# Kernel optimization log

Measured on AMD Instinct MI355X. Metric: run time of the kernel, lower is better.

Reference implementation:

```python
import math
import jax, jax.numpy as jnp
import numpy as np

SHAPES = [(80, 80), (40, 40), (20, 20), (10, 10)]
BS, LQ, D, NH, NL, NP = 8, 1000, 256, 8, 4, 4
C = D // NH


def _offset_bias():
    # replicates _reset_parameters grid_init bias for sampling_offsets
    thetas = np.arange(NH, dtype=np.float32) * (2.0 * math.pi / NH)
    grid = np.stack([np.cos(thetas), np.sin(thetas)], -1)  # [NH,2]
    grid = grid / np.abs(grid).max(-1, keepdims=True)
    grid = np.tile(grid[:, None, None, :], (1, NL, NP, 1))  # [NH,NL,NP,2]
    for i in range(NP):
        grid[:, :, i, :] *= i + 1
    return jnp.asarray(grid.reshape(-1))


def setup_inputs() -> dict:
    key = jax.random.key(0)
    ks = jax.random.split(key, 8)
    len_v = sum(h * w for h, w in SHAPES)
    s = 1.0 / math.sqrt(D)
    starts = np.cumsum([0] + [h * w for h, w in SHAPES])[:-1]
    return {
        "query": jax.random.normal(ks[0], (BS, LQ, D), jnp.float32),
        "reference_points": jax.random.uniform(ks[1], (BS, LQ, NL, 2), jnp.float32),
        "value": jax.random.normal(ks[2], (BS, len_v, D), jnp.float32),
        "w_off": jax.random.normal(ks[3], (D, NH * NL * NP * 2), jnp.float32) * 0.01,
        "b_off": _offset_bias(),
        "w_attn": jax.random.normal(ks[4], (D, NH * NL * NP), jnp.float32) * 0.01,
        "b_attn": jnp.zeros((NH * NL * NP,), jnp.float32),
        "w_v": jax.random.normal(ks[5], (D, D), jnp.float32) * s,
        "b_v": jnp.zeros((D,), jnp.float32),
        "w_o": jax.random.normal(ks[6], (D, D), jnp.float32) * s,
        "b_o": jnp.zeros((D,), jnp.float32),
        "value_spatial_shapes": jnp.array(SHAPES, jnp.int32),
        "value_level_start_index": jnp.array(starts, jnp.int32),
    }


def _sample(img, grid, H, W):
    # bilinear grid_sample, padding_mode='zeros', align_corners=False
    # img: [B, C, H*W], grid: [B, Q, P, 2] in [-1, 1] -> out [B, C, Q, P]
    x = (grid[..., 0] + 1.0) * (W * 0.5) - 0.5
    y = (grid[..., 1] + 1.0) * (H * 0.5) - 0.5
    x0 = jnp.floor(x)
    y0 = jnp.floor(y)
    fx = x - x0
    fy = y - y0
    x0i = x0.astype(jnp.int32)
    y0i = y0.astype(jnp.int32)

    def gather(xi, yi, w):
        valid = (xi >= 0) & (xi < W) & (yi >= 0) & (yi < H)
        idx = jnp.clip(yi, 0, H - 1) * W + jnp.clip(xi, 0, W - 1)
        B, Q, P = idx.shape
        g = jax.vmap(lambda im, ix: im[:, ix])(img, idx.reshape(B, Q * P))  # [B,C,QP]
        return g.reshape(B, -1, Q, P) * (w * valid)[:, None]

    return (gather(x0i, y0i, (1 - fx) * (1 - fy))
            + gather(x0i + 1, y0i, fx * (1 - fy))
            + gather(x0i, y0i + 1, (1 - fx) * fy)
            + gather(x0i + 1, y0i + 1, fx * fy))


def _forward(query, reference_points, value, w_off, b_off, w_attn, b_attn,
             w_v, b_v, w_o, b_o, shapes):
    bs, lq, _ = query.shape
    v = (value @ w_v + b_v).reshape(bs, -1, NH, C)  # [bs, len_v, NH, C]
    off = (query @ w_off + b_off).reshape(bs, lq, NH, NL, NP, 2)
    attn = jax.nn.softmax((query @ w_attn + b_attn).reshape(bs, lq, NH, NL * NP), axis=-1)
    attn = attn.reshape(bs, lq, NH, NL, NP)
    # offset normalizer is spatial_shapes flipped -> (W, H) per level
    norm = jnp.array([[w, h] for h, w in shapes], dtype=query.dtype)  # [NL,2]
    loc = reference_points[:, :, None, :, None, :] + off / norm[None, None, None, :, None, :]
    grids = 2.0 * loc - 1.0  # [bs,lq,NH,NL,NP,2]
    start = 0
    sampled = []
    for lvl, (H, W) in enumerate(shapes):
        v_l = v[:, start:start + H * W].transpose(0, 2, 3, 1).reshape(bs * NH, C, H * W)
        g_l = grids[:, :, :, lvl].transpose(0, 2, 1, 3, 4).reshape(bs * NH, lq, NP, 2)
        sampled.append(_sample(v_l, g_l, H, W))  # [bs*NH, C, lq, NP]
        start += H * W
    samp = jnp.stack(sampled, axis=3).reshape(bs * NH, C, lq, NL * NP)
    aw = attn.transpose(0, 2, 1, 3, 4).reshape(bs * NH, 1, lq, NL * NP)
    out = (samp * aw).sum(-1).reshape(bs, NH * C, lq).transpose(0, 2, 1)  # [bs,lq,D]
    return out @ w_o + b_o


def reference(query, reference_points, value, w_off, b_off, w_attn, b_attn,
              w_v, b_v, w_o, b_o, value_spatial_shapes, value_level_start_index):
    shapes = [tuple(int(x) for x in r) for r in np.asarray(value_spatial_shapes)]
    return _forward(query, reference_points, value, w_off, b_off, w_attn, b_attn,
                    w_v, b_v, w_o, b_o, shapes)
```

## Files before the change

kernel.cpp:

```cpp
#include <hip/hip_runtime.h>
#include <hip/hip_bf16.h>
#include <math.h>

#define BS     8
#define LQ     1000
#define DMODEL 256
#define NH     8
#define NLV    4
#define NPT    4
#define LEN_V  8500
#define NQ     (BS*LQ)
#define MV     (BS*LEN_V)
#define KS     8

typedef __attribute__((ext_vector_type(8))) short short8;
typedef __attribute__((ext_vector_type(4))) float floatx4;

static __device__ __forceinline__ unsigned short f2bf(float f) {
    __hip_bfloat16 h = __float2bfloat16(f);
    return __builtin_bit_cast(unsigned short, h);
}
static __device__ __forceinline__ float asf(unsigned int u) {
    return __builtin_bit_cast(float, u);
}

static __device__ __forceinline__ void dma16(const unsigned short* g, unsigned short* lds) {
    __builtin_amdgcn_global_load_lds(
        (const __attribute__((address_space(1))) unsigned int*)g,
        (__attribute__((address_space(3))) unsigned int*)lds,
        16, 0, 0);
}

static __device__ __forceinline__ void gemm_dma_core(
    const unsigned short* __restrict__ Ab, const unsigned short* __restrict__ Bfrag,
    const float* __restrict__ bias1, const float* __restrict__ bias2, int nsplit,
    void* __restrict__ Cptr, int M, int N, int bn, int bm_start, int bm_stride,
    bool outbf, unsigned short (*As)[16384])
{
    const int tid = threadIdx.x;
    const int l   = tid & 63;
    const int w   = tid >> 6;
    const int lm  = l & 15;
    const int lk  = l >> 4;
    const int x7  = lm & 7;
    const int n_mtiles = (M + 63) >> 6;

    short8 Bf[2][KS];
    const int u0 = bn * 8 + w * 2;
    #pragma unroll
    for (int j = 0; j < 2; ++j)
        #pragma unroll
        for (int s = 0; s < KS; ++s)
            Bf[j][s] = *(const short8*)(Bfrag + ((size_t)((u0 + j) * KS + s) * 64 + l) * 8);

    auto dma_tile = [&](int tile, int buf) {
        #pragma unroll
        for (int j = 0; j < 8; ++j) {
            const int slot = j * 256 + tid;
            const int row  = slot >> 5;
            const int gp   = slot & 31;
            const int gc   = gp ^ (row & 7);
            int grow = tile * 64 + row; grow = grow < M ? grow : M - 1;
            dma16(Ab + (size_t)grow * 256 + gc * 8,
                  &As[buf][(j * 256 + w * 64) * 8]);
        }
    };

    int bm  = bm_start;
    int buf = 0;
    if (bm < n_mtiles) dma_tile(bm, 0);

    while (bm < n_mtiles) {
        const int bm_next = bm + bm_stride;

        __builtin_amdgcn_s_waitcnt(0);
        __syncthreads();
        if (bm_next < n_mtiles) dma_tile(bm_next, buf ^ 1);

        floatx4 acc[4][2];
        #pragma unroll
        for (int i = 0; i < 4; ++i)
            #pragma unroll
            for (int j = 0; j < 2; ++j)
                #pragma unroll
                for (int r = 0; r < 4; ++r) acc[i][j][r] = 0.f;

        #pragma unroll
        for (int s = 0; s < KS; ++s) {
            short8 afr[4];
            #pragma unroll
            for (int i = 0; i < 4; ++i)
                afr[i] = *(const short8*)(
                    &As[buf][(i * 16 + lm) * 256 + (((s * 4 + lk) ^ x7)) * 8]);
            #pragma unroll
            for (int i = 0; i < 4; ++i)
                #pragma unroll
                for (int j = 0; j < 2; ++j)
                    acc[i][j] = __builtin_amdgcn_mfma_f32_16x16x32_bf16(
                                    afr[i], Bf[j][s], acc[i][j], 0, 0, 0);
        }

        #pragma unroll
        for (int j = 0; j < 2; ++j) {
            const int col = bn * 128 + w * 32 + j * 16 + lm;
            const float bv = (bias2 != nullptr && col >= nsplit) ? bias2[col - nsplit]
                                                                 : bias1[col];
            #pragma unroll
            for (int i = 0; i < 4; ++i) {
                const int rbase = bm * 64 + i * 16 + lk * 4;
                #pragma unroll
                for (int r = 0; r < 4; ++r) {
                    const int row = rbase + r;
                    if (row < M) {
                        const float v = acc[i][j][r] + bv;
                        if (outbf)
                            ((unsigned short*)Cptr)[(size_t)row * N + col] = f2bf(v);
                        else
                            ((float*)Cptr)[(size_t)row * N + col] = v;
                    }
                }
            }
        }

        buf ^= 1;
        bm = bm_next;
    }
}

__global__ __launch_bounds__(256, 2) void gemm_fused(
    const unsigned short* __restrict__ valq_bf,
    const unsigned short* __restrict__ wv_f, const unsigned short* __restrict__ woa_f,
    const float* __restrict__ b_v, const float* __restrict__ b_off,
    const float* __restrict__ b_attn,
    unsigned short* __restrict__ v_proj, float* __restrict__ offattn)
{
    __shared__ unsigned short As[2][16384];
    int bx = blockIdx.x;
    if (bx < 1064) {
        const int bm0 = bx % 532, bn = bx / 532;
        gemm_dma_core(valq_bf, wv_f, b_v, nullptr, 1 << 30,
                      v_proj, MV, 256, bn, bm0, 532, true, As);
    } else {
        bx -= 1064;
        const int bm0 = bx % 125, bn = bx / 125;
        gemm_dma_core(valq_bf + (size_t)MV * 256, woa_f, b_off, b_attn, 256,
                      offattn, NQ, 384, bn, bm0, 125, false, As);
    }
}

__global__ __launch_bounds__(256, 2) void gemm_out(
    const unsigned short* __restrict__ out_pre, const unsigned short* __restrict__ wo_f,
    const float* __restrict__ b_o, float* __restrict__ out)
{
    __shared__ unsigned short As[2][16384];
    gemm_dma_core(out_pre, wo_f, b_o, nullptr, 1 << 30,
                  out, NQ, 256, blockIdx.y, blockIdx.x, 125, false, As);
}

__global__ __launch_bounds__(256) void prep(
    const float* __restrict__ value, const float* __restrict__ query,
    unsigned short* __restrict__ valq_bf,
    const float* __restrict__ w_v, const float* __restrict__ w_off,
    const float* __restrict__ w_attn, const float* __restrict__ w_o,
    unsigned short* __restrict__ wv_f, unsigned short* __restrict__ woa_f,
    unsigned short* __restrict__ wo_f)
{
    const int bx = blockIdx.x;
    if (bx < 19000) {
        const int i = bx * 256 + threadIdx.x;
        const float4 v = (i < 4352000) ? ((const float4*)value)[i]
                                       : ((const float4*)query)[i - 4352000];
        ushort4 o;
        o.x = f2bf(v.x); o.y = f2bf(v.y); o.z = f2bf(v.z); o.w = f2bf(v.w);
        ((ushort4*)valq_bf)[i] = o;
    } else {
        const int gid = (bx - 19000) * 256 + threadIdx.x;
        int chunk, mode;
        if (gid < 8192)               { chunk = gid;         mode = 0; }
        else if (gid < 8192 + 12288)  { chunk = gid - 8192;  mode = 1; }
        else                          { chunk = gid - 20480; mode = 2; }
        const int l = chunk & 63, s = (chunk >> 6) & 7, u = chunk >> 9;
        short8 o;
        #pragma unroll
        for (int j = 0; j < 8; ++j) {
            const int k = s * 32 + (l >> 4) * 8 + j;
            const int n = u * 16 + (l & 15);
            float v;
            if (mode == 0)      v = w_v[k * 256 + n];
            else if (mode == 1) v = (n < 256) ? w_off[k * 256 + n] : w_attn[k * 128 + (n - 256)];
            else                v = w_o[k * 256 + n];
            o[j] = (short)f2bf(v);
        }
        unsigned short* dp = (mode == 0 ? wv_f : mode == 1 ? woa_f : wo_f)
                             + ((size_t)(u * 8 + s) * 64 + l) * 8;
        *(short8*)dp = o;
    }
}

__global__ __launch_bounds__(512) void ms_sample_split(
    const unsigned short* __restrict__ v,
    const float* __restrict__ offattn,
    const float* __restrict__ refp,
    unsigned short* __restrict__ out_pre)
{
    __shared__ float offx_s[8][16][8];
    __shared__ float offy_s[8][16][8];
    __shared__ float atw_s [8][16][8];
    __shared__ float ref_s [8][8];
    __shared__ float part  [8][32][9];

    const int tid  = threadIdx.x;
    const int bswz = blockIdx.x & 7;
    const int iq0  = bswz * 1000 + (blockIdx.x >> 3) * 8;

    if (tid < 64) {
        const int q = tid >> 3, h = tid & 7;
        const float* rowp = offattn + (size_t)(iq0 + q) * 384;
        float lg[16];
        float m = -1e30f;
        #pragma unroll
        for (int i = 0; i < 16; ++i) { lg[i] = rowp[256 + h * 16 + i]; m = fmaxf(m, lg[i]); }
        float s = 0.f;
        #pragma unroll
        for (int i = 0; i < 16; ++i) { lg[i] = __expf(lg[i] - m); s += lg[i]; }
        const float inv = 1.f / s;
        #pragma unroll
        for (int i = 0; i < 16; ++i) atw_s[q][i][h] = lg[i] * inv;
        #pragma unroll
        for (int i = 0; i < 16; ++i) {
            offx_s[q][i][h] = rowp[(h * 16 + i) * 2 + 0];
            offy_s[q][i][h] = rowp[(h * 16 + i) * 2 + 1];
        }
        if (h == 0) {
            #pragma unroll
            for (int i = 0; i < 8; ++i) ref_s[q][i] = refp[(size_t)(iq0 + q) * 8 + i];
        }
    }
    __syncthreads();

    const int q8   = tid >> 6;
    const int half = (tid >> 5) & 1;
    const int sub  = tid & 31;
    const int h    = sub >> 2;
    const int oct  = sub & 3;

    float acc[8] = {0.f, 0.f, 0.f, 0.f, 0.f, 0.f, 0.f, 0.f};
    const unsigned short* vb = v + (size_t)bswz * LEN_V * 256 + h * 32 + oct * 8;
    const int Hs[4] = {80, 40, 20, 10};
    const int st[4] = {0, 6400, 8000, 8400};

    #pragma unroll
    for (int li = 0; li < 2; ++li) {
        const int lvl = half * 2 + li;
        const int W = Hs[lvl];
        const float bx = ref_s[q8][lvl * 2 + 0] * (float)W - 0.5f;
        const float by = ref_s[q8][lvl * 2 + 1] * (float)W - 0.5f;
        const unsigned short* vl = vb + (size_t)st[lvl] * 256;
        #pragma unroll
        for (int p = 0; p < NPT; ++p) {
            const int lp = lvl * 4 + p;
            const float x  = bx + offx_s[q8][lp][h];
            const float y  = by + offy_s[q8][lp][h];
            const float at = atw_s[q8][lp][h];
            const float x0f = floorf(x), y0f = floorf(y);
            const float fx = x - x0f, fy = y - y0f;
            const int x0 = (int)x0f, y0 = (int)y0f;
            const int x1 = x0 + 1,   y1 = y0 + 1;
            const int cx0 = min(max(x0, 0), W - 1);
            const int cx1 = min(max(x1, 0), W - 1);
            const int cy0 = min(max(y0, 0), W - 1);
            const int cy1 = min(max(y1, 0), W - 1);
            const float vx0 = (x0 >= 0 && x0 < W) ? 1.f : 0.f;
            const float vx1 = (x1 >= 0 && x1 < W) ? 1.f : 0.f;
            const float vy0 = (y0 >= 0 && y0 < W) ? 1.f : 0.f;
            const float vy1 = (y1 >= 0 && y1 < W) ? 1.f : 0.f;
            const float w00 = at * (1.f - fx) * (1.f - fy) * vx0 * vy0;
            const float w01 = at * fx * (1.f - fy) * vx1 * vy0;
            const float w10 = at * (1.f - fx) * fy * vx0 * vy1;
            const float w11 = at * fx * fy * vx1 * vy1;
            const unsigned short* r0 = vl + (size_t)(cy0 * W) * 256;
            const unsigned short* r1 = vl + (size_t)(cy1 * W) * 256;
            const uint4 d00 = *(const uint4*)(r0 + (size_t)cx0 * 256);
            const uint4 d01 = *(const uint4*)(r0 + (size_t)cx1 * 256);
            const uint4 d10 = *(const uint4*)(r1 + (size_t)cx0 * 256);
            const uint4 d11 = *(const uint4*)(r1 + (size_t)cx1 * 256);
            acc[0] += w00 * asf(d00.x << 16) + w01 * asf(d01.x << 16)
                    + w10 * asf(d10.x << 16) + w11 * asf(d11.x << 16);
            acc[1] += w00 * asf(d00.x & 0xffff0000u) + w01 * asf(d01.x & 0xffff0000u)
                    + w10 * asf(d10.x & 0xffff0000u) + w11 * asf(d11.x & 0xffff0000u);
            acc[2] += w00 * asf(d00.y << 16) + w01 * asf(d01.y << 16)
                    + w10 * asf(d10.y << 16) + w11 * asf(d11.y << 16);
            acc[3] += w00 * asf(d00.y & 0xffff0000u) + w01 * asf(d01.y & 0xffff0000u)
                    + w10 * asf(d10.y & 0xffff0000u) + w11 * asf(d11.y & 0xffff0000u);
            acc[4] += w00 * asf(d00.z << 16) + w01 * asf(d01.z << 16)
                    + w10 * asf(d10.z << 16) + w11 * asf(d11.z << 16);
            acc[5] += w00 * asf(d00.z & 0xffff0000u) + w01 * asf(d01.z & 0xffff0000u)
                    + w10 * asf(d10.z & 0xffff0000u) + w11 * asf(d11.z & 0xffff0000u);
            acc[6] += w00 * asf(d00.w << 16) + w01 * asf(d01.w << 16)
                    + w10 * asf(d10.w << 16) + w11 * asf(d11.w << 16);
            acc[7] += w00 * asf(d00.w & 0xffff0000u) + w01 * asf(d01.w & 0xffff0000u)
                    + w10 * asf(d10.w & 0xffff0000u) + w11 * asf(d11.w & 0xffff0000u);
        }
    }

    if (half == 1) {
        #pragma unroll
        for (int j = 0; j < 8; ++j) part[q8][sub][j] = acc[j];
    }
    __syncthreads();
    if (half == 0) {
        short8 o;
        #pragma unroll
        for (int j = 0; j < 8; ++j) o[j] = (short)f2bf(acc[j] + part[q8][sub][j]);
        *(short8*)(out_pre + (size_t)(iq0 + q8) * 256 + sub * 8) = o;
    }
}

extern "C" void kernel_launch(void* const* d_in, const int* in_sizes, int n_in,
                              void* d_out, int out_size, void* d_ws, size_t ws_size,
                              hipStream_t stream)
{
    const float* query  = (const float*)d_in[0];
    const float* refp   = (const float*)d_in[1];
    const float* value  = (const float*)d_in[2];
    const float* w_off  = (const float*)d_in[3];
    const float* b_off  = (const float*)d_in[4];
    const float* w_attn = (const float*)d_in[5];
    const float* b_attn = (const float*)d_in[6];
    const float* w_v    = (const float*)d_in[7];
    const float* b_v    = (const float*)d_in[8];
    const float* w_o    = (const float*)d_in[9];
    const float* b_o    = (const float*)d_in[10];
    (void)d_in[11]; (void)d_in[12];

    float* out = (float*)d_out;

    char* ws = (char*)d_ws;
    unsigned short* valq_bf = (unsigned short*)ws;
    unsigned short* out_pre = (unsigned short*)ws;
    unsigned short* v_proj  = (unsigned short*)(ws + 38912000);
    float*          offattn = (float*)(ws + 73728000);
    unsigned short* wv_f    = (unsigned short*)(ws + 86016000);
    unsigned short* woa_f   = (unsigned short*)(ws + 86147072);
    unsigned short* wo_f    = (unsigned short*)(ws + 86343680);

    dim3 blk(256);

    hipLaunchKernelGGL(prep, dim3(19112), blk, 0, stream,
                       value, query, valq_bf, w_v, w_off, w_attn, w_o,
                       wv_f, woa_f, wo_f);
    hipLaunchKernelGGL(gemm_fused, dim3(1439), blk, 0, stream,
                       valq_bf, wv_f, woa_f, b_v, b_off, b_attn, v_proj, offattn);
    hipLaunchKernelGGL(ms_sample_split, dim3(1000), dim3(512), 0, stream,
                       v_proj, offattn, refp, out_pre);
    hipLaunchKernelGGL(gemm_out, dim3(125, 2), blk, 0, stream,
                       out_pre, wo_f, b_o, out);
}
```

Before: 192.3 us.

## Fuse fp32-to-bf16 activation conversion into projection GEMM tile loads

Removes the standalone pass that converted value and query to bf16 in workspace. The projection GEMM now loads fp32 tiles into registers, converts them to bf16 and stores them swizzled into LDS, prefetching the next tile in registers. This eliminates a large write/read round trip of converted activations and one big launch. In exchange the GEMM reads twice the bytes per tile, loses the async global-to-LDS DMA path, and uses more registers.

```diff
diff --git a/kernel.cpp b/kernel.cpp
--- a/kernel.cpp
+++ b/kernel.cpp
@@ -31,8 +31,9 @@
         16, 0, 0);
 }
 
-static __device__ __forceinline__ void gemm_dma_core(
-    const unsigned short* __restrict__ Ab, const unsigned short* __restrict__ Bfrag,
+template <bool A32>
+static __device__ __forceinline__ void gemm_core(
+    const void* __restrict__ Aptr, const unsigned short* __restrict__ Bfrag,
     const float* __restrict__ bias1, const float* __restrict__ bias2, int nsplit,
     void* __restrict__ Cptr, int M, int N, int bn, int bm_start, int bm_stride,
     bool outbf, unsigned short (*As)[16384])
@@ -53,29 +54,67 @@
         for (int s = 0; s < KS; ++s)
             Bf[j][s] = *(const short8*)(Bfrag + ((size_t)((u0 + j) * KS + s) * 64 + l) * 8);
 
-    auto dma_tile = [&](int tile, int buf) {
-        #pragma unroll
-        for (int j = 0; j < 8; ++j) {
-            const int slot = j * 256 + tid;
-            const int row  = slot >> 5;
-            const int gp   = slot & 31;
-            const int gc   = gp ^ (row & 7);
-            int grow = tile * 64 + row; grow = grow < M ? grow : M - 1;
-            dma16(Ab + (size_t)grow * 256 + gc * 8,
-                  &As[buf][(j * 256 + w * 64) * 8]);
-        }
+    auto aoff = [&](int tile, int j) -> size_t {
+        const int slot = j * 256 + tid;
+        const int row  = slot >> 5;
+        const int gc   = (slot & 31) ^ (row & 7);
+        int grow = tile * 64 + row; grow = grow < M ? grow : M - 1;
+        return (size_t)grow * 256 + gc * 8;
     };
+
+    float4 ra[8][2];
 
     int bm  = bm_start;
     int buf = 0;
-    if (bm < n_mtiles) dma_tile(bm, 0);
+    if (bm < n_mtiles) {
+        if constexpr (A32) {
+            #pragma unroll
+            for (int j = 0; j < 8; ++j) {
+                const float* s = (const float*)Aptr + aoff(bm, j);
+                ra[j][0] = *(const float4*)s;
+                ra[j][1] = *(const float4*)(s + 4);
+            }
+        } else {
+            #pragma unroll
+            for (int j = 0; j < 8; ++j)
+                dma16((const unsigned short*)Aptr + aoff(bm, j),
+                      &As[0][(j * 256 + w * 64) * 8]);
+        }
+    }
 
     while (bm < n_mtiles) {
         const int bm_next = bm + bm_stride;
 
-        __builtin_amdgcn_s_waitcnt(0);
-        __syncthreads();
-        if (bm_next < n_mtiles) dma_tile(bm_next, buf ^ 1);
+        if constexpr (A32) {
+            #pragma unroll
+            for (int j = 0; j < 8; ++j) {
+                const int slot = j * 256 + tid;
+                short8 o;
+                o[0] = (short)f2bf(ra[j][0].x); o[1] = (short)f2bf(ra[j][0].y);
+                o[2] = (short)f2bf(ra[j][0].z); o[3] = (short)f2bf(ra[j][0].w);
+                o[4] = (short)f2bf(ra[j][1].x); o[5] = (short)f2bf(ra[j][1].y);
+                o[6] = (short)f2bf(ra[j][1].z); o[7] = (short)f2bf(ra[j][1].w);
+                *(short8*)&As[buf][slot * 8] = o;
+            }
+            if (bm_next < n_mtiles) {
+                #pragma unroll
+                for (int j = 0; j < 8; ++j) {
+                    const float* s = (const float*)Aptr + aoff(bm_next, j);
+                    ra[j][0] = *(const float4*)s;
+                    ra[j][1] = *(const float4*)(s + 4);
+                }
+            }
+            __syncthreads();
+        } else {
+            __builtin_amdgcn_s_waitcnt(0);
+            __syncthreads();
+            if (bm_next < n_mtiles) {
+                #pragma unroll
+                for (int j = 0; j < 8; ++j)
+                    dma16((const unsigned short*)Aptr + aoff(bm_next, j),
+                          &As[buf ^ 1][(j * 256 + w * 64) * 8]);
+            }
+        }
 
         floatx4 acc[4][2];
         #pragma unroll
@@ -128,7 +167,7 @@
 }
 
 __global__ __launch_bounds__(256, 2) void gemm_fused(
-    const unsigned short* __restrict__ valq_bf,
+    const float* __restrict__ value, const float* __restrict__ query,
     const unsigned short* __restrict__ wv_f, const unsigned short* __restrict__ woa_f,
     const float* __restrict__ b_v, const float* __restrict__ b_off,
     const float* __restrict__ b_attn,
@@ -138,13 +177,13 @@
     int bx = blockIdx.x;
     if (bx < 1064) {
         const int bm0 = bx % 532, bn = bx / 532;
-        gemm_dma_core(valq_bf, wv_f, b_v, nullptr, 1 << 30,
-                      v_proj, MV, 256, bn, bm0, 532, true, As);
+        gemm_core<true>(value, wv_f, b_v, nullptr, 1 << 30,
+                        v_proj, MV, 256, bn, bm0, 532, true, As);
     } else {
         bx -= 1064;
         const int bm0 = bx % 125, bn = bx / 125;
-        gemm_dma_core(valq_bf + (size_t)MV * 256, woa_f, b_off, b_attn, 256,
-                      offattn, NQ, 384, bn, bm0, 125, false, As);
+        gemm_core<true>(query, woa_f, b_off, b_attn, 256,
+                        offattn, NQ, 384, bn, bm0, 125, false, As);
     }
 }
 
@@ -153,48 +192,36 @@
     const float* __restrict__ b_o, float* __restrict__ out)
 {
     __shared__ unsigned short As[2][16384];
-    gemm_dma_core(out_pre, wo_f, b_o, nullptr, 1 << 30,
-                  out, NQ, 256, blockIdx.y, blockIdx.x, 125, false, As);
-}
-
-__global__ __launch_bounds__(256) void prep(
-    const float* __restrict__ value, const float* __restrict__ query,
-    unsigned short* __restrict__ valq_bf,
+    gemm_core<false>(out_pre, wo_f, b_o, nullptr, 1 << 30,
+                     out, NQ, 256, blockIdx.y, blockIdx.x, 125, false, As);
+}
+
+__global__ __launch_bounds__(256) void prep_w(
     const float* __restrict__ w_v, const float* __restrict__ w_off,
     const float* __restrict__ w_attn, const float* __restrict__ w_o,
     unsigned short* __restrict__ wv_f, unsigned short* __restrict__ woa_f,
     unsigned short* __restrict__ wo_f)
 {
-    const int bx = blockIdx.x;
-    if (bx < 19000) {
-        const int i = bx * 256 + threadIdx.x;
-        const float4 v = (i < 4352000) ? ((const float4*)value)[i]
-                                       : ((const float4*)query)[i - 4352000];
-        ushort4 o;
-        o.x = f2bf(v.x); o.y = f2bf(v.y); o.z = f2bf(v.z); o.w = f2bf(v.w);
-        ((ushort4*)valq_bf)[i] = o;
-    } else {
-        const int gid = (bx - 19000) * 256 + threadIdx.x;
-        int chunk, mode;
-        if (gid < 8192)               { chunk = gid;         mode = 0; }
-        else if (gid < 8192 + 12288)  { chunk = gid - 8192;  mode = 1; }
-        else                          { chunk = gid - 20480; mode = 2; }
-        const int l = chunk & 63, s = (chunk >> 6) & 7, u = chunk >> 9;
-        short8 o;
-        #pragma unroll
-        for (int j = 0; j < 8; ++j) {
-            const int k = s * 32 + (l >> 4) * 8 + j;
-            const int n = u * 16 + (l & 15);
-            float v;
-            if (mode == 0)      v = w_v[k * 256 + n];
-            else if (mode == 1) v = (n < 256) ? w_off[k * 256 + n] : w_attn[k * 128 + (n - 256)];
-            else                v = w_o[k * 256 + n];
-            o[j] = (short)f2bf(v);
-        }
-        unsigned short* dp = (mode == 0 ? wv_f : mode == 1 ? woa_f : wo_f)
-                             + ((size_t)(u * 8 + s) * 64 + l) * 8;
-        *(short8*)dp = o;
-    }
+    const int gid = blockIdx.x * 256 + threadIdx.x;
+    int chunk, mode;
+    if (gid < 8192)               { chunk = gid;         mode = 0; }
+    else if (gid < 8192 + 12288)  { chunk = gid - 8192;  mode = 1; }
+    else                          { chunk = gid - 20480; mode = 2; }
+    const int l = chunk & 63, s = (chunk >> 6) & 7, u = chunk >> 9;
+    short8 o;
+    #pragma unroll
+    for (int j = 0; j < 8; ++j) {
+        const int k = s * 32 + (l >> 4) * 8 + j;
+        const int n = u * 16 + (l & 15);
+        float v;
+        if (mode == 0)      v = w_v[k * 256 + n];
+        else if (mode == 1) v = (n < 256) ? w_off[k * 256 + n] : w_attn[k * 128 + (n - 256)];
+        else                v = w_o[k * 256 + n];
+        o[j] = (short)f2bf(v);
+    }
+    unsigned short* dp = (mode == 0 ? wv_f : mode == 1 ? woa_f : wo_f)
+                         + ((size_t)(u * 8 + s) * 64 + l) * 8;
+    *(short8*)dp = o;
 }
 
 __global__ __launch_bounds__(512) void ms_sample_split(
@@ -336,21 +363,19 @@
     float* out = (float*)d_out;
 
     char* ws = (char*)d_ws;
-    unsigned short* valq_bf = (unsigned short*)ws;
-    unsigned short* out_pre = (unsigned short*)ws;
-    unsigned short* v_proj  = (unsigned short*)(ws + 38912000);
-    float*          offattn = (float*)(ws + 73728000);
-    unsigned short* wv_f    = (unsigned short*)(ws + 86016000);
-    unsigned short* woa_f   = (unsigned short*)(ws + 86147072);
-    unsigned short* wo_f    = (unsigned short*)(ws + 86343680);
+    unsigned short* v_proj  = (unsigned short*)ws;
+    float*          offattn = (float*)(ws + 34816000);
+    unsigned short* out_pre = (unsigned short*)(ws + 47104000);
+    unsigned short* wv_f    = (unsigned short*)(ws + 51200000);
+    unsigned short* woa_f   = (unsigned short*)(ws + 51331072);
+    unsigned short* wo_f    = (unsigned short*)(ws + 51527680);
 
     dim3 blk(256);
 
-    hipLaunchKernelGGL(prep, dim3(19112), blk, 0, stream,
-                       value, query, valq_bf, w_v, w_off, w_attn, w_o,
-                       wv_f, woa_f, wo_f);
+    hipLaunchKernelGGL(prep_w, dim3(112), blk, 0, stream,
+                       w_v, w_off, w_attn, w_o, wv_f, woa_f, wo_f);
     hipLaunchKernelGGL(gemm_fused, dim3(1439), blk, 0, stream,
-                       valq_bf, wv_f, woa_f, b_v, b_off, b_attn, v_proj, offattn);
+                       value, query, wv_f, woa_f, b_v, b_off, b_attn, v_proj, offattn);
     hipLaunchKernelGGL(ms_sample_split, dim3(1000), dim3(512), 0, stream,
                        v_proj, offattn, refp, out_pre);
     hipLaunchKernelGGL(gemm_out, dim3(125, 2), blk, 0, stream,
```

Measured after the change: 197.1 us. 2.5% more time.
